# Performance work log

Measured on AMD Instinct MI355X. Metric: run time of the kernel, lower is better.

Reference implementation:

```python
import jax, jax.numpy as jnp
import numpy as np

N_HEAD = 16
N_STATE = 1024
NEG_INF = -1e9


def setup_inputs() -> dict:
    key = jax.random.key(0)
    k1, = jax.random.split(key, 1)
    B, S = 4, 2048
    x = jax.random.normal(k1, (B, S, 3 * N_STATE), dtype=jnp.float32)
    # causal attention mask (1 = keep, 0 = masked), broadcast over heads
    attn_mask = jnp.tril(jnp.ones((S, S), dtype=jnp.float32))[None, None, :, :]
    attn_mask = jnp.broadcast_to(attn_mask, (B, 1, S, S))
    return {"x": x, "attn_mask": attn_mask}


def reference(x, attn_mask) -> jnp.ndarray:
    B, S, _ = x.shape
    d_head = N_STATE // N_HEAD
    q = x[:, :, :N_STATE].reshape(B, S, N_HEAD, d_head).transpose(0, 2, 1, 3)  # [B,H,S,D]
    k = x[:, :, N_STATE:2 * N_STATE].reshape(B, S, N_HEAD, d_head).transpose(0, 2, 1, 3)
    v = x[:, :, 2 * N_STATE:].reshape(B, S, N_HEAD, d_head).transpose(0, 2, 1, 3)
    scale = 1.0 / jnp.sqrt(jnp.asarray(d_head, dtype=x.dtype))
    w = jnp.einsum('bhqd,bhkd->bhqk', q, k) * scale           # [B,H,S,S]
    w = attn_mask * w + (1.0 - attn_mask) * NEG_INF
    w = jax.nn.softmax(w, axis=-1)
    # attention_dropout is identity at inference (Keras Dropout, training=False)
    a = jnp.einsum('bhqk,bhkd->bhqd', w, v)                   # [B,H,S,D]
    return a.transpose(0, 2, 1, 3).reshape(B, S, N_STATE)
```

## Files before the change

### kernel.cpp

```cpp
#include <hip/hip_runtime.h>


typedef float  f32x4  __attribute__((ext_vector_type(4)));
typedef short  bf16x8 __attribute__((ext_vector_type(8)));

#define NH      16
#define DH      64
#define SEQ     2048
#define NSTATE  1024
#define ROW3    3072
#define BQ      128
#define BK      64
#define NQB     (SEQ / BQ)
#define KST     72
#define VST     72
#define PST     72
#define NEG_BIG (-1e9f)
#define QSC     (0.125f * 1.4426950408889634f)

static __device__ __forceinline__ unsigned pk2(float x, float y) {
    unsigned ux = __builtin_bit_cast(unsigned, x);
    unsigned uy = __builtin_bit_cast(unsigned, y);
    ux += 0x7FFFu + ((ux >> 16) & 1u);
    uy += 0x7FFFu + ((uy >> 16) & 1u);
    return __builtin_amdgcn_perm(uy, ux, 0x07060302u);
}

__global__ __launch_bounds__(512, 4)
void mha_fwd(const float* __restrict__ x, float* __restrict__ out) {
    const int tid  = threadIdx.x;
    const int wave = tid >> 6;
    const int lane = tid & 63;
    const int l16  = lane & 15;
    const int quad = lane >> 4;

    const int pr = blockIdx.x;
    const int bh = blockIdx.y;
    const int b  = bh >> 4;
    const int h  = bh & 15;

    const float* xb    = x + (size_t)b * SEQ * ROW3;
    const float* kbase = xb + NSTATE + h * DH;
    const float* vbase = xb + 2 * NSTATE + h * DH;
    float*       ob    = out + (size_t)b * SEQ * NSTATE + h * DH;

    __shared__ __align__(16) short Klds[BK * KST];
    __shared__ __align__(16) short Vlds[DH * VST];
    __shared__ __align__(16) short Plds[8][16 * PST];

    bf16x8 vones;
#pragma unroll
    for (int i = 0; i < 8; ++i) vones[i] = (short)0x3F80;

#pragma unroll 1
    for (int ph = 0; ph < 2; ++ph) {
        const int qblk = ph ? (NQB - 1 - pr) : pr;
        const int q0   = qblk * BQ;
        const int qmin = q0 + wave * 16;
        const int qrow = qmin + l16;

        bf16x8 qf[2];
        {
            const float* qp = xb + (size_t)qrow * ROW3 + h * DH + quad * 8;
#pragma unroll
            for (int f = 0; f < 2; ++f) {
                float4 a = *(const float4*)(qp + 32 * f);
                float4 c = *(const float4*)(qp + 32 * f + 4);
                union { bf16x8 v; unsigned u[4]; } qq;
                qq.u[0] = pk2(a.x * QSC, a.y * QSC);
                qq.u[1] = pk2(a.z * QSC, a.w * QSC);
                qq.u[2] = pk2(c.x * QSC, c.y * QSC);
                qq.u[3] = pk2(c.z * QSC, c.w * QSC);
                qf[f] = qq.v;
            }
        }

        f32x4 o[4];
#pragma unroll
        for (int t = 0; t < 4; ++t) o[t] = (f32x4){0.f, 0.f, 0.f, 0.f};
        f32x4 ol = (f32x4){0.f, 0.f, 0.f, 0.f};

        const int ntiles = q0 / BK + BQ / BK;
#pragma unroll 1
        for (int it = 0; it < ntiles; ++it) {
            const int kv0 = it * BK;
            __syncthreads();

#pragma unroll
            for (int i = 0; i < 2; ++i) {
                int p  = tid + 512 * i;
                int kv = p >> 4;
                int d  = (p & 15) * 4;
                const float* gp = kbase + (size_t)(kv0 + kv) * ROW3 + d;
                float4 v = *(const float4*)gp;
                uint2 pk;
                pk.x = pk2(v.x, v.y);
                pk.y = pk2(v.z, v.w);
                *(uint2*)&Klds[kv * KST + d] = pk;
            }
#pragma unroll
            for (int i = 0; i < 4; ++i) {
                int idx = tid + 512 * i;
                int d   = idx & 63;
                int kv  = (idx >> 6) * 2;
                const float* gp = vbase + (size_t)(kv0 + kv) * ROW3 + d;
                float v0 = gp[0];
                float v1 = gp[ROW3];
                *(unsigned*)&Vlds[d * VST + kv] = pk2(v0, v1);
            }
            __syncthreads();

            if (kv0 > qmin + 15) continue;

            bf16x8 kf[4][2];
#pragma unroll
            for (int t = 0; t < 4; ++t)
#pragma unroll
                for (int f = 0; f < 2; ++f)
                    kf[t][f] = *(const bf16x8*)&Klds[(16 * t + l16) * KST + quad * 8 + 32 * f];
            bf16x8 vf[4][2];
#pragma unroll
            for (int t = 0; t < 4; ++t)
#pragma unroll
                for (int f = 0; f < 2; ++f)
                    vf[t][f] = *(const bf16x8*)&Vlds[(16 * t + l16) * VST + quad * 8 + 32 * f];

            f32x4 sc[4];
#pragma unroll
            for (int t = 0; t < 4; ++t) {
                f32x4 c = (f32x4){0.f, 0.f, 0.f, 0.f};
                c = __builtin_amdgcn_mfma_f32_16x16x32_bf16(kf[t][0], qf[0], c, 0, 0, 0);
                c = __builtin_amdgcn_mfma_f32_16x16x32_bf16(kf[t][1], qf[1], c, 0, 0, 0);
                sc[t] = c;
            }
            if (kv0 + BK - 1 > qmin) {
#pragma unroll
                for (int t = 0; t < 4; ++t)
#pragma unroll
                    for (int r = 0; r < 4; ++r) {
                        int kvg = kv0 + 16 * t + 4 * quad + r;
                        if (kvg > qrow) sc[t][r] = NEG_BIG;
                    }
            }

#pragma unroll
            for (int t = 0; t < 4; ++t)
#pragma unroll
                for (int r = 0; r < 4; ++r)
                    sc[t][r] = __builtin_amdgcn_exp2f(sc[t][r]);

            short* pb = &Plds[wave][0];
#pragma unroll
            for (int t = 0; t < 4; ++t) {
                uint2 pk;
                pk.x = pk2(sc[t][0], sc[t][1]);
                pk.y = pk2(sc[t][2], sc[t][3]);
                *(uint2*)&pb[l16 * PST + 16 * t + 4 * quad] = pk;
            }
            __asm__ volatile("s_waitcnt lgkmcnt(0)" ::: "memory");
            bf16x8 pf0 = *(const bf16x8*)&pb[l16 * PST + quad * 8];
            bf16x8 pf1 = *(const bf16x8*)&pb[l16 * PST + quad * 8 + 32];

#pragma unroll
            for (int t = 0; t < 4; ++t) {
                f32x4 c = o[t];
                c = __builtin_amdgcn_mfma_f32_16x16x32_bf16(pf0, vf[t][0], c, 0, 0, 0);
                c = __builtin_amdgcn_mfma_f32_16x16x32_bf16(pf1, vf[t][1], c, 0, 0, 0);
                o[t] = c;
            }
            ol = __builtin_amdgcn_mfma_f32_16x16x32_bf16(pf0, vones, ol, 0, 0, 0);
            ol = __builtin_amdgcn_mfma_f32_16x16x32_bf16(pf1, vones, ol, 0, 0, 0);
        }

        {
            const int qtop = qmin + 4 * quad;
            float lr[4];
#pragma unroll
            for (int r = 0; r < 4; ++r) lr[r] = 1.0f / ol[r];
#pragma unroll
            for (int t = 0; t < 4; ++t)
#pragma unroll
                for (int r = 0; r < 4; ++r)
                    ob[(size_t)(qtop + r) * NSTATE + 16 * t + l16] = o[t][r] * lr[r];
        }
    }
}

extern "C" void kernel_launch(void* const* d_in, const int* in_sizes, int n_in,
                              void* d_out, int out_size, void* d_ws, size_t ws_size,
                              hipStream_t stream) {
    const float* x = (const float*)d_in[0];
    float* out = (float*)d_out;
    dim3 grid(NQB / 2, 4 * NH);
    dim3 block(512);
    hipLaunchKernelGGL(mha_fwd, grid, block, 0, stream, x, out);
}
```

Measured before the change: 254.1 us.

## Pre-convert K/V to swizzled bf16 in workspace and async-load tiles into LDS

Adds a prep kernel that converts K to bf16 and V to transposed bf16, both with XOR-swizzled layouts, and writes them into the workspace. The attention kernel then moves tiles straight from global memory to LDS with global_load_lds, with no per-tile fp32 conversion or strided V gathers. Query blocks shrink to 64 rows, run as 256-thread blocks, so the grid has more blocks and masked work on the diagonal tile is smaller. This costs an extra launch and a pass through 32 MB of workspace; the old kernel is kept as a fallback when the workspace is too small.

New measurement: 261.6 us. 1.03x slower.

```diff
diff --git a/kernel.cpp b/kernel.cpp
--- a/kernel.cpp
+++ b/kernel.cpp
@@ -9,14 +9,9 @@
 #define SEQ     2048
 #define NSTATE  1024
 #define ROW3    3072
-#define BQ      128
-#define BK      64
-#define NQB     (SEQ / BQ)
-#define KST     72
-#define VST     72
-#define PST     72
 #define NEG_BIG (-1e9f)
 #define QSC     (0.125f * 1.4426950408889634f)
+#define WS_NEED (33554432u)
 
 static __device__ __forceinline__ unsigned pk2(float x, float y) {
     unsigned ux = __builtin_bit_cast(unsigned, x);
@@ -25,28 +20,100 @@
     uy += 0x7FFFu + ((uy >> 16) & 1u);
     return __builtin_amdgcn_perm(uy, ux, 0x07060302u);
 }
-
-__global__ __launch_bounds__(512, 4)
-void mha_fwd(const float* __restrict__ x, float* __restrict__ out) {
+static __device__ __forceinline__ short b1(float x) {
+    unsigned u = __builtin_bit_cast(unsigned, x);
+    u += 0x7FFFu + ((u >> 16) & 1u);
+    return (short)(u >> 16);
+}
+static __device__ __forceinline__ void async16(const void* g, void* l) {
+    __builtin_amdgcn_global_load_lds(
+        (const __attribute__((address_space(1))) unsigned*)g,
+        (__attribute__((address_space(3))) unsigned*)l, 16, 0, 0);
+}
+
+__global__ __launch_bounds__(256)
+void qkv_prep(const float* __restrict__ x, short* __restrict__ kbf,
+              short* __restrict__ vt) {
+    const int tid   = threadIdx.x;
+    const int stile = blockIdx.x;
+    const int bh    = blockIdx.y;
+    const int b = bh >> 4, h = bh & 15;
+    const int s0 = stile * 64;
+
+    const float* kg = x + (size_t)b * SEQ * ROW3 + NSTATE + h * DH;
+    const float* vg = x + (size_t)b * SEQ * ROW3 + 2 * NSTATE + h * DH;
+
+    __shared__ short T[64 * 66];
+
+    unsigned* kout = (unsigned*)kbf + ((size_t)bh * SEQ + s0) * 32;
+#pragma unroll
+    for (int j = 0; j < 4; ++j) {
+        int idx = tid + 256 * j;
+        int s   = idx >> 4;
+        int dq  = (idx & 15) * 4;
+        float4 v = *(const float4*)(kg + (size_t)(s0 + s) * ROW3 + dq);
+        unsigned lo = pk2(v.x, v.y), hi = pk2(v.z, v.w);
+        int cp = (dq >> 3) ^ (s & 7);
+        unsigned* o = kout + s * 32 + cp * 4 + ((dq & 7) >> 1);
+        o[0] = lo; o[1] = hi;
+    }
+#pragma unroll
+    for (int j = 0; j < 4; ++j) {
+        int idx = tid + 256 * j;
+        int s   = idx >> 4;
+        int dq  = (idx & 15) * 4;
+        float4 v = *(const float4*)(vg + (size_t)(s0 + s) * ROW3 + dq);
+        T[(dq + 0) * 66 + s] = b1(v.x);
+        T[(dq + 1) * 66 + s] = b1(v.y);
+        T[(dq + 2) * 66 + s] = b1(v.z);
+        T[(dq + 3) * 66 + s] = b1(v.w);
+    }
+    __syncthreads();
+    {
+        unsigned* vout = (unsigned*)vt + (size_t)bh * DH * (SEQ / 2) + (s0 >> 1);
+        int d  = tid >> 2;
+        int sc = (tid & 3) * 16;
+        unsigned r[8];
+#pragma unroll
+        for (int k = 0; k < 8; ++k)
+            r[k] = *(const unsigned*)&T[d * 66 + sc + k * 2];
+        int c0  = sc >> 3;
+        int c0p = c0 ^ (d & 7);
+        int c1p = (c0 + 1) ^ (d & 7);
+        uint4 w0 = {r[0], r[1], r[2], r[3]};
+        uint4 w1 = {r[4], r[5], r[6], r[7]};
+        *(uint4*)(vout + (size_t)d * (SEQ / 2) + c0p * 4) = w0;
+        *(uint4*)(vout + (size_t)d * (SEQ / 2) + c1p * 4) = w1;
+    }
+}
+
+#define BQ2   64
+#define NQB2  (SEQ / BQ2)
+#define PST   72
+
+__global__ __launch_bounds__(256, 4)
+void mha_core(const float* __restrict__ x, const short* __restrict__ kbf,
+              const short* __restrict__ vt, float* __restrict__ out) {
     const int tid  = threadIdx.x;
     const int wave = tid >> 6;
     const int lane = tid & 63;
     const int l16  = lane & 15;
     const int quad = lane >> 4;
+    const int sw   = l16 & 7;
 
     const int pr = blockIdx.x;
     const int bh = blockIdx.y;
     const int b  = bh >> 4;
     const int h  = bh & 15;
 
-    const float* xb    = x + (size_t)b * SEQ * ROW3;
-    const float* kbase = xb + NSTATE + h * DH;
-    const float* vbase = xb + 2 * NSTATE + h * DH;
-    float*       ob    = out + (size_t)b * SEQ * NSTATE + h * DH;
-
-    __shared__ __align__(16) short Klds[BK * KST];
-    __shared__ __align__(16) short Vlds[DH * VST];
-    __shared__ __align__(16) short Plds[8][16 * PST];
+    const float* xb = x + (size_t)b * SEQ * ROW3;
+    float*       ob = out + (size_t)b * SEQ * NSTATE + h * DH;
+    const char*  kgb = (const char*)kbf + (size_t)bh * SEQ * 128;
+    const char*  vgb = (const char*)vt + (size_t)bh * DH * SEQ * 2;
+
+    __shared__ __align__(16) short Klds[64 * 64];
+    __shared__ __align__(16) short Vlds[64 * 64];
+    __shared__ __align__(16) short Plds[4][16 * PST];
 
     bf16x8 vones;
 #pragma unroll
@@ -54,8 +121,8 @@
 
 #pragma unroll 1
     for (int ph = 0; ph < 2; ++ph) {
-        const int qblk = ph ? (NQB - 1 - pr) : pr;
-        const int q0   = qblk * BQ;
+        const int qblk = ph ? (NQB2 - 1 - pr) : pr;
+        const int q0   = qblk * BQ2;
         const int qmin = q0 + wave * 16;
         const int qrow = qmin + l16;
 
@@ -80,12 +147,163 @@
         for (int t = 0; t < 4; ++t) o[t] = (f32x4){0.f, 0.f, 0.f, 0.f};
         f32x4 ol = (f32x4){0.f, 0.f, 0.f, 0.f};
 
+        const int nt = q0 / 64 + 1;
+#pragma unroll 1
+        for (int it = 0; it < nt; ++it) {
+            const int kv0 = it * 64;
+            __syncthreads();
+
+            {
+                const char* kt = kgb + (size_t)kv0 * 128;
+                const char* vtt = vgb + (size_t)kv0 * 2;
+#pragma unroll
+                for (int j = 0; j < 2; ++j) {
+                    int seg = wave * 2 + j;
+                    async16(kt + seg * 1024 + lane * 16,
+                            (char*)Klds + seg * 1024);
+                    int d = seg * 8 + (lane >> 3);
+                    async16(vtt + (size_t)d * 4096 + (lane & 7) * 16,
+                            (char*)Vlds + seg * 1024);
+                }
+            }
+            __syncthreads();
+
+            bf16x8 kf[4][2], vf[4][2];
+#pragma unroll
+            for (int t = 0; t < 4; ++t)
+#pragma unroll
+                for (int f = 0; f < 2; ++f) {
+                    int off = (16 * t + l16) * 128 + (((quad + 4 * f) ^ sw) * 16);
+                    kf[t][f] = *(const bf16x8*)((const char*)Klds + off);
+                    vf[t][f] = *(const bf16x8*)((const char*)Vlds + off);
+                }
+
+            f32x4 sc[4];
+#pragma unroll
+            for (int t = 0; t < 4; ++t) {
+                f32x4 c = (f32x4){0.f, 0.f, 0.f, 0.f};
+                c = __builtin_amdgcn_mfma_f32_16x16x32_bf16(kf[t][0], qf[0], c, 0, 0, 0);
+                c = __builtin_amdgcn_mfma_f32_16x16x32_bf16(kf[t][1], qf[1], c, 0, 0, 0);
+                sc[t] = c;
+            }
+            if (it == nt - 1) {
+#pragma unroll
+                for (int t = 0; t < 4; ++t)
+#pragma unroll
+                    for (int r = 0; r < 4; ++r) {
+                        int kvg = kv0 + 16 * t + 4 * quad + r;
+                        if (kvg > qrow) sc[t][r] = NEG_BIG;
+                    }
+            }
+
+#pragma unroll
+            for (int t = 0; t < 4; ++t)
+#pragma unroll
+                for (int r = 0; r < 4; ++r)
+                    sc[t][r] = __builtin_amdgcn_exp2f(sc[t][r]);
+
+            short* pb = &Plds[wave][0];
+#pragma unroll
+            for (int t = 0; t < 4; ++t) {
+                uint2 pk;
+                pk.x = pk2(sc[t][0], sc[t][1]);
+                pk.y = pk2(sc[t][2], sc[t][3]);
+                *(uint2*)&pb[l16 * PST + 16 * t + 4 * quad] = pk;
+            }
+            __asm__ volatile("s_waitcnt lgkmcnt(0)" ::: "memory");
+            bf16x8 pf0 = *(const bf16x8*)&pb[l16 * PST + quad * 8];
+            bf16x8 pf1 = *(const bf16x8*)&pb[l16 * PST + quad * 8 + 32];
+
+#pragma unroll
+            for (int t = 0; t < 4; ++t) {
+                f32x4 c = o[t];
+                c = __builtin_amdgcn_mfma_f32_16x16x32_bf16(pf0, vf[t][0], c, 0, 0, 0);
+                c = __builtin_amdgcn_mfma_f32_16x16x32_bf16(pf1, vf[t][1], c, 0, 0, 0);
+                o[t] = c;
+            }
+            ol = __builtin_amdgcn_mfma_f32_16x16x32_bf16(pf0, vones, ol, 0, 0, 0);
+            ol = __builtin_amdgcn_mfma_f32_16x16x32_bf16(pf1, vones, ol, 0, 0, 0);
+        }
+
+        {
+            const int qtop = qmin + 4 * quad;
+            float lr[4];
+#pragma unroll
+            for (int r = 0; r < 4; ++r) lr[r] = 1.0f / ol[r];
+#pragma unroll
+            for (int t = 0; t < 4; ++t)
+#pragma unroll
+                for (int r = 0; r < 4; ++r)
+                    ob[(size_t)(qtop + r) * NSTATE + 16 * t + l16] = o[t][r] * lr[r];
+        }
+    }
+}
+
+#define BQ      128
+#define BK      64
+#define NQB     (SEQ / BQ)
+#define KST     72
+#define VST     72
+
+__global__ __launch_bounds__(512, 4)
+void mha_fwd_r4(const float* __restrict__ x, float* __restrict__ out) {
+    const int tid  = threadIdx.x;
+    const int wave = tid >> 6;
+    const int lane = tid & 63;
+    const int l16  = lane & 15;
+    const int quad = lane >> 4;
+
+    const int pr = blockIdx.x;
+    const int bh = blockIdx.y;
+    const int b  = bh >> 4;
+    const int h  = bh & 15;
+
+    const float* xb    = x + (size_t)b * SEQ * ROW3;
+    const float* kbase = xb + NSTATE + h * DH;
+    const float* vbase = xb + 2 * NSTATE + h * DH;
+    float*       ob    = out + (size_t)b * SEQ * NSTATE + h * DH;
+
+    __shared__ __align__(16) short Klds[BK * KST];
+    __shared__ __align__(16) short Vlds[DH * VST];
+    __shared__ __align__(16) short Plds[8][16 * PST];
+
+    bf16x8 vones;
+#pragma unroll
+    for (int i = 0; i < 8; ++i) vones[i] = (short)0x3F80;
+
+#pragma unroll 1
+    for (int ph = 0; ph < 2; ++ph) {
+        const int qblk = ph ? (NQB - 1 - pr) : pr;
+        const int q0   = qblk * BQ;
+        const int qmin = q0 + wave * 16;
+        const int qrow = qmin + l16;
+
+        bf16x8 qf[2];
+        {
+            const float* qp = xb + (size_t)qrow * ROW3 + h * DH + quad * 8;
+#pragma unroll
+            for (int f = 0; f < 2; ++f) {
+                float4 a = *(const float4*)(qp + 32 * f);
+                float4 c = *(const float4*)(qp + 32 * f + 4);
+                union { bf16x8 v; unsigned u[4]; } qq;
+                qq.u[0] = pk2(a.x * QSC, a.y * QSC);
+                qq.u[1] = pk2(a.z * QSC, a.w * QSC);
+                qq.u[2] = pk2(c.x * QSC, c.y * QSC);
+                qq.u[3] = pk2(c.z * QSC, c.w * QSC);
+                qf[f] = qq.v;
+            }
+        }
+
+        f32x4 o[4];
+#pragma unroll
+        for (int t = 0; t < 4; ++t) o[t] = (f32x4){0.f, 0.f, 0.f, 0.f};
+        f32x4 ol = (f32x4){0.f, 0.f, 0.f, 0.f};
+
         const int ntiles = q0 / BK + BQ / BK;
 #pragma unroll 1
         for (int it = 0; it < ntiles; ++it) {
             const int kv0 = it * BK;
             __syncthreads();
-
 #pragma unroll
             for (int i = 0; i < 2; ++i) {
                 int p  = tid + 512 * i;
@@ -104,26 +322,20 @@
                 int d   = idx & 63;
                 int kv  = (idx >> 6) * 2;
                 const float* gp = vbase + (size_t)(kv0 + kv) * ROW3 + d;
-                float v0 = gp[0];
-                float v1 = gp[ROW3];
-                *(unsigned*)&Vlds[d * VST + kv] = pk2(v0, v1);
+                *(unsigned*)&Vlds[d * VST + kv] = pk2(gp[0], gp[ROW3]);
             }
             __syncthreads();
 
             if (kv0 > qmin + 15) continue;
 
-            bf16x8 kf[4][2];
-#pragma unroll
-            for (int t = 0; t < 4; ++t)
-#pragma unroll
-                for (int f = 0; f < 2; ++f)
+            bf16x8 kf[4][2], vf[4][2];
+#pragma unroll
+            for (int t = 0; t < 4; ++t)
+#pragma unroll
+                for (int f = 0; f < 2; ++f) {
                     kf[t][f] = *(const bf16x8*)&Klds[(16 * t + l16) * KST + quad * 8 + 32 * f];
-            bf16x8 vf[4][2];
-#pragma unroll
-            for (int t = 0; t < 4; ++t)
-#pragma unroll
-                for (int f = 0; f < 2; ++f)
                     vf[t][f] = *(const bf16x8*)&Vlds[(16 * t + l16) * VST + quad * 8 + 32 * f];
+                }
 
             f32x4 sc[4];
 #pragma unroll
@@ -142,7 +354,6 @@
                         if (kvg > qrow) sc[t][r] = NEG_BIG;
                     }
             }
-
 #pragma unroll
             for (int t = 0; t < 4; ++t)
 #pragma unroll
@@ -171,7 +382,6 @@
             ol = __builtin_amdgcn_mfma_f32_16x16x32_bf16(pf0, vones, ol, 0, 0, 0);
             ol = __builtin_amdgcn_mfma_f32_16x16x32_bf16(pf1, vones, ol, 0, 0, 0);
         }
-
         {
             const int qtop = qmin + 4 * quad;
             float lr[4];
@@ -191,7 +401,15 @@
                               hipStream_t stream) {
     const float* x = (const float*)d_in[0];
     float* out = (float*)d_out;
-    dim3 grid(NQB / 2, 4 * NH);
-    dim3 block(512);
-    hipLaunchKernelGGL(mha_fwd, grid, block, 0, stream, x, out);
-}
+    if (ws_size >= WS_NEED) {
+        short* kbf = (short*)d_ws;
+        short* vt  = (short*)((char*)d_ws + WS_NEED / 2);
+        hipLaunchKernelGGL(qkv_prep, dim3(SEQ / 64, 4 * NH), dim3(256), 0, stream,
+                           x, kbf, vt);
+        hipLaunchKernelGGL(mha_core, dim3(NQB2 / 2, 4 * NH), dim3(256), 0, stream,
+                           x, kbf, vt, out);
+    } else {
+        hipLaunchKernelGGL(mha_fwd_r4, dim3(NQB / 2, 4 * NH), dim3(512), 0, stream,
+                           x, out);
+    }
+}
```
